# Optimization experiments

Measured on AMD Instinct MI355X. Metric: run time of the kernel, lower is better.

## Reference

```python
import jax, jax.numpy as jnp
import numpy as np

D = 256  # model dim, used for 1/sqrt(d) scaling


def setup_inputs() -> dict:
    key = jax.random.key(0)
    ks = jax.random.split(key, 6)
    B, N, Dm, K = 4, 8192, 256, 256
    s = 0.02
    return {
        "I": jax.random.normal(ks[0], (B, N, Dm), dtype=jnp.float32),
        "Wq": jax.random.normal(ks[1], (Dm, Dm), dtype=jnp.float32) * s,
        "Wk": jax.random.normal(ks[2], (Dm, Dm), dtype=jnp.float32) * s,
        "Wv": jax.random.normal(ks[3], (Dm, Dm), dtype=jnp.float32) * s,
        "We": jax.random.normal(ks[4], (K, N), dtype=jnp.float32) * s,
        "Wf": jax.random.normal(ks[5], (K, N), dtype=jnp.float32) * s,
    }


def reference(I, Wq, Wk, Wv, We, Wf):
    # I: [B, n, d]; nn.Linear applies x @ W.T
    Q = jnp.einsum("bnd,ed->bne", I, Wq)          # [B, n, d]
    K = jnp.einsum("bnd,ed->bne", I, Wk)          # [B, n, d]
    V = jnp.einsum("bnd,ed->bne", I, Wv)          # [B, n, d]
    # E projects K along the sequence axis: K^T [B,d,n] -> [B,d,k]
    Ke = jnp.einsum("bnd,kn->bdk", K, We)         # [B, d, k]
    # F projects V along the sequence axis, then transpose back: [B,k,d]
    Vf = jnp.einsum("bnd,kn->bkd", V, Wf)         # [B, k, d]
    scale = 1.0 / jnp.sqrt(jnp.asarray(D, dtype=Q.dtype))
    PBar = jnp.einsum("bnd,bdk->bnk", Q, Ke) * scale  # [B, n, k]
    PBar = jax.nn.softmax(PBar, axis=2)
    # dropout omitted (eval / deterministic reference)
    Head = jnp.einsum("bnk,bkd->bnd", PBar, Vf)   # [B, n, d]
    return Head
```

## Files before the change

### kernel.cpp

```cpp
#include <hip/hip_runtime.h>
#include <stdint.h>


typedef unsigned short u16;
typedef __attribute__((ext_vector_type(8))) __bf16 bf16x8;
typedef __attribute__((ext_vector_type(4))) float f32x4;
typedef __attribute__((ext_vector_type(4))) unsigned short u16x4;
typedef __attribute__((ext_vector_type(8))) unsigned short u16x8;

__device__ __forceinline__ u16 f2bf(float f) {
  union { __bf16 h; u16 u; } v;
  v.h = (__bf16)f;
  return v.u;
}

__device__ __forceinline__ void gld_lds16(const void* g, void* l) {
  __builtin_amdgcn_global_load_lds((const __attribute__((address_space(1))) void*)g,
                                   (__attribute__((address_space(3))) void*)l, 16, 0, 0);
}

__device__ __forceinline__ void stage_tile(const u16* src, long long ld, long long kb,
                                           u16* lds, int tid) {
#pragma unroll
  for (int r = 0; r < 4; ++r) {
    const int off = r * 4096 + tid * 16;
    const int row = off >> 7;
    const int colb = (off & 127) ^ ((row & 7) << 4);
    gld_lds16(src + (long long)row * ld + kb + (colb >> 1), (char*)lds + off);
  }
}

__device__ __forceinline__ void mfma_step(const u16* Alds, const u16* Blds, int lane, int wr,
                                          int wc, f32x4 (&acc)[4][4]) {
#pragma unroll
  for (int kk = 0; kk < 2; ++kk) {
    const int ko2 = (kk * 32 + (lane >> 4) * 8) * 2;
    bf16x8 a[4], b[4];
#pragma unroll
    for (int m = 0; m < 4; ++m) {
      const int ar = wr + m * 16 + (lane & 15);
      a[m] = *(const bf16x8*)((const char*)Alds + ((ar * 128 + ko2) ^ ((ar & 7) << 4)));
    }
#pragma unroll
    for (int n = 0; n < 4; ++n) {
      const int br = wc + n * 16 + (lane & 15);
      b[n] = *(const bf16x8*)((const char*)Blds + ((br * 128 + ko2) ^ ((br & 7) << 4)));
    }
#pragma unroll
    for (int m = 0; m < 4; ++m)
#pragma unroll
      for (int n = 0; n < 4; ++n)
        acc[m][n] = __builtin_amdgcn_mfma_f32_16x16x32_bf16(a[m], b[n], acc[m][n], 0, 0, 0);
  }
}

__global__ __launch_bounds__(256) void k0(const float* __restrict__ I,
                                          const float* __restrict__ Wq,
                                          const float* __restrict__ Wk,
                                          const float* __restrict__ Wv,
                                          const float* __restrict__ We,
                                          const float* __restrict__ Wf,
                                          u16* __restrict__ Ibf, u16* __restrict__ IT,
                                          u16* __restrict__ WqT, u16* __restrict__ WkT,
                                          u16* __restrict__ WvB, u16* __restrict__ WeB,
                                          u16* __restrict__ WfB) {
  const int p = blockIdx.x, t = threadIdx.x;
  if (p < 2080) {
    __shared__ u16 T[4096];
    const float* src;
    u16 *dT, *dS;
    long long srow, scol, tld;
    if (p < 2048) {
      const int b = p >> 9, id = p & 511;
      src = I + (long long)b * 2097152;
      srow = (long long)(id >> 2) * 64;
      scol = (long long)(id & 3) * 64;
      dS = Ibf + (long long)b * 2097152;
      dT = IT + (long long)b * 2097152;
      tld = 8192;
    } else {
      const int q = p - 2048;
      src = (q < 16) ? Wq : Wk;
      const int id = q & 15;
      srow = (long long)(id >> 2) * 64;
      scol = (long long)(id & 3) * 64;
      dS = nullptr;
      dT = (q < 16) ? WqT : WkT;
      tld = 256;
    }
    const int cc = t & 15, rL = t >> 4;
#pragma unroll
    for (int i = 0; i < 4; ++i) {
      const int r = rL + 16 * i;
      f32x4 v = *(const f32x4*)(src + (srow + r) * 256 + scol + cc * 4);
      u16x4 o = {f2bf(v[0]), f2bf(v[1]), f2bf(v[2]), f2bf(v[3])};
      if (dS) *(u16x4*)(dS + (srow + r) * 256 + scol + cc * 4) = o;
      const int P = (cc + (r & 15) + 4 * (r >> 4)) & 15;
      *(u16x4*)&T[r * 64 + P * 4] = o;
    }
    __syncthreads();
    const int dd = t >> 2, ch2 = t & 3;
    u16 buf[16];
#pragma unroll
    for (int j = 0; j < 16; ++j) {
      const int P = ((dd >> 2) + j + 4 * ch2) & 15;
      buf[j] = T[(ch2 * 16 + j) * 64 + P * 4 + (dd & 3)];
    }
    u16* dp = dT + (scol + dd) * tld + srow + ch2 * 16;
    *(u16x8*)dp = *(u16x8*)&buf[0];
    *(u16x8*)(dp + 8) = *(u16x8*)&buf[8];
  } else {
    const long long base = (long long)(p - 2080) * 4096;
#pragma unroll
    for (int rnd = 0; rnd < 4; ++rnd) {
      const long long e = base + rnd * 1024 + t * 4;
      const float* s;
      u16* d;
      long long eo;
      if (e < 65536) { s = Wv; d = WvB; eo = e; }
      else if (e < 2162688) { s = We; d = WeB; eo = e - 65536; }
      else { s = Wf; d = WfB; eo = e - 2162688; }
      f32x4 v = *(const f32x4*)(s + eo);
      *(u16x4*)(d + eo) = u16x4{f2bf(v[0]), f2bf(v[1]), f2bf(v[2]), f2bf(v[3])};
    }
  }
}

__global__ __launch_bounds__(256) void k1(const u16* __restrict__ WqT,
                                          const u16* __restrict__ WkT,
                                          const u16* __restrict__ WeB,
                                          const u16* __restrict__ WfB,
                                          const u16* __restrict__ IT,
                                          float* __restrict__ Pp, u16* __restrict__ G) {
  __shared__ u16 Alds[2][8192];
  __shared__ u16 Blds[2][8192];
  const int tid = threadIdx.x, lane = tid & 63, w = tid >> 6;
  const int wr = (w >> 1) * 64, wc = (w & 1) * 64;
  const u16 *A, *Bp;
  long long lda, k0, crow, ccol;
  int nkt;
  float* Cf = nullptr;
  u16* Cb = nullptr;
  if (blockIdx.x >= 512) {
    const int tl = blockIdx.x - 512;
    crow = (long long)(tl >> 1) * 128;
    ccol = (long long)(tl & 1) * 128;
    A = WqT + crow * 256;
    Bp = WkT + ccol * 256;
    lda = 256; k0 = 0; nkt = 4;
    Cb = G;
  } else {
    const int l = ((blockIdx.x & 7) << 6) + (blockIdx.x >> 3);
    const int mT = l & 1, nT = (l >> 1) & 1, s = (l >> 2) & 15, b = (l >> 6) & 3, op = l >> 8;
    A = (op ? WfB : WeB) + (long long)mT * 128 * 8192;
    Bp = IT + (long long)b * 2097152 + (long long)nT * 128 * 8192;
    lda = 8192;
    k0 = (long long)s * 512;
    nkt = 8;
    Cf = Pp + ((long long)(op * 4 + b) * 16 + s) * 65536;
    crow = (long long)mT * 128;
    ccol = (long long)nT * 128;
  }

  f32x4 acc[4][4];
#pragma unroll
  for (int m = 0; m < 4; ++m)
#pragma unroll
    for (int n = 0; n < 4; ++n) acc[m][n] = f32x4{0.f, 0.f, 0.f, 0.f};

  stage_tile(A, lda, k0, Alds[0], tid);
  stage_tile(Bp, lda, k0, Blds[0], tid);
  __syncthreads();
  int cur = 0;
  for (int kt = 0; kt < nkt; ++kt) {
    if (kt + 1 < nkt) {
      stage_tile(A, lda, k0 + (kt + 1) * 64, Alds[cur ^ 1], tid);
      stage_tile(Bp, lda, k0 + (kt + 1) * 64, Blds[cur ^ 1], tid);
    }
    mfma_step(Alds[cur], Blds[cur], lane, wr, wc, acc);
    __syncthreads();
    cur ^= 1;
  }

  const int r0 = (lane >> 4) * 4, c0 = lane & 15;
#pragma unroll
  for (int m = 0; m < 4; ++m)
#pragma unroll
    for (int n = 0; n < 4; ++n) {
      const long long row = crow + wr + m * 16 + r0;
      const long long col = ccol + wc + n * 16 + c0;
#pragma unroll
      for (int j = 0; j < 4; ++j) {
        if (Cf) Cf[(row + j) * 256 + col] = acc[m][n][j];
        else Cb[(row + j) * 256 + col] = f2bf(acc[m][n][j]);
      }
    }
}

__global__ __launch_bounds__(256) void reduce16(const float* __restrict__ P,
                                                u16* __restrict__ O) {
  const long long t = (long long)blockIdx.x * 256 + threadIdx.x;
  const long long g = t >> 14;
  const long long e = (t & 16383) << 2;
  const float* p = P + g * 1048576 + e;
  f32x4 s = {0.f, 0.f, 0.f, 0.f};
#pragma unroll
  for (int i = 0; i < 16; ++i) s += *(const f32x4*)(p + i * 65536);
  u16x4 o = {f2bf(s[0]), f2bf(s[1]), f2bf(s[2]), f2bf(s[3])};
  *(u16x4*)(O + g * 65536 + e) = o;
}

__global__ __launch_bounds__(256) void k3(const u16* __restrict__ SS, const u16* __restrict__ G,
                                          const u16* __restrict__ WvB, u16* __restrict__ Me,
                                          u16* __restrict__ VfT) {
  __shared__ u16 Alds[2][8192];
  __shared__ u16 Blds[2][8192];
  const int tid = threadIdx.x, lane = tid & 63, w = tid >> 6;
  const int wr = (w >> 1) * 64, wc = (w & 1) * 64;
  const int u = blockIdx.x;
  const int path = u >> 4, b = (u >> 2) & 3, mT = (u >> 1) & 1, nT = u & 1;
  const u16 *A, *Bp;
  u16* C;
  if (path == 0) { A = SS + b * 65536; Bp = G; C = Me + b * 65536; }
  else { A = WvB; Bp = SS + (4 + b) * 65536; C = VfT + b * 65536; }
  A += (long long)mT * 128 * 256;
  Bp += (long long)nT * 128 * 256;

  f32x4 acc[4][4];
#pragma unroll
  for (int m = 0; m < 4; ++m)
#pragma unroll
    for (int n = 0; n < 4; ++n) acc[m][n] = f32x4{0.f, 0.f, 0.f, 0.f};

  stage_tile(A, 256, 0, Alds[0], tid);
  stage_tile(Bp, 256, 0, Blds[0], tid);
  __syncthreads();
  int cur = 0;
  for (int kt = 0; kt < 4; ++kt) {
    if (kt + 1 < 4) {
      stage_tile(A, 256, (kt + 1) * 64, Alds[cur ^ 1], tid);
      stage_tile(Bp, 256, (kt + 1) * 64, Blds[cur ^ 1], tid);
    }
    mfma_step(Alds[cur], Blds[cur], lane, wr, wc, acc);
    __syncthreads();
    cur ^= 1;
  }

  const int r0 = (lane >> 4) * 4, c0 = lane & 15;
#pragma unroll
  for (int m = 0; m < 4; ++m)
#pragma unroll
    for (int n = 0; n < 4; ++n) {
      const int row = mT * 128 + wr + m * 16 + r0;
      const int col = nT * 128 + wc + n * 16 + c0;
#pragma unroll
      for (int j = 0; j < 4; ++j) C[(row + j) * 256 + col] = f2bf(acc[m][n][j]);
    }
}

__device__ __forceinline__ void stage_bs(const u16* src, u16* Bs, int tid) {
#pragma unroll
  for (int r = 0; r < 8; ++r) {
    const int off = r * 4096 + tid * 16;
    const int row = off >> 7;
    const int colb = (off & 127) ^ ((row & 7) << 4);
    gld_lds16(src + row * 256 + (colb >> 1), (char*)Bs + off);
  }
}

__global__ __launch_bounds__(256) void flash3(const u16* __restrict__ Q,
                                              const u16* __restrict__ KeT,
                                              const u16* __restrict__ VfT,
                                              float* __restrict__ out) {
  __shared__ u16 Qs[16384];
  __shared__ u16 Bs[16384];
  __shared__ float Ms[256];
  __shared__ float Ss[256];
  const int tid = threadIdx.x;
  const int lane = tid & 63;
  const int w = tid >> 6;
  const int wc = w * 64;
  const int l = ((blockIdx.x & 7) << 6) + (blockIdx.x >> 3);
  const long long R0 = (long long)l * 64;
  const int batch = (int)(R0 >> 13);
  const u16* KeTb = KeT + (long long)batch * 65536;
  const u16* VfTb = VfT + (long long)batch * 65536;
  const int r0 = (lane >> 4) * 4, c0 = lane & 15;

#pragma unroll
  for (int r = 0; r < 8; ++r) {
    const int off = r * 4096 + tid * 16;
    const int row = off >> 9;
    const int colb = (off & 511) ^ ((row & 7) << 4);
    gld_lds16(Q + (R0 + row) * 256 + (colb >> 1), (char*)Qs + off);
  }

  f32x4 acc[4][4];
#pragma unroll
  for (int m = 0; m < 4; ++m)
#pragma unroll
    for (int n = 0; n < 4; ++n) acc[m][n] = f32x4{0.f, 0.f, 0.f, 0.f};

  for (int kc = 0; kc < 4; ++kc) {
    __syncthreads();
    stage_bs(KeTb + kc * 64, Bs, tid);
    __syncthreads();
#pragma unroll
    for (int kk = 0; kk < 2; ++kk) {
      const int ko = kk * 32 + (lane >> 4) * 8;
      bf16x8 a[4], b[4];
#pragma unroll
      for (int m = 0; m < 4; ++m) {
        const int ar = m * 16 + (lane & 15);
        a[m] = *(const bf16x8*)((const char*)Qs +
                                ((ar * 512 + (kc * 64 + ko) * 2) ^ ((ar & 7) << 4)));
      }
#pragma unroll
      for (int n = 0; n < 4; ++n) {
        const int br = wc + n * 16 + (lane & 15);
        b[n] = *(const bf16x8*)((const char*)Bs + ((br * 128 + ko * 2) ^ ((br & 7) << 4)));
      }
#pragma unroll
      for (int m = 0; m < 4; ++m)
#pragma unroll
        for (int n = 0; n < 4; ++n)
          acc[m][n] = __builtin_amdgcn_mfma_f32_16x16x32_bf16(a[m], b[n], acc[m][n], 0, 0, 0);
    }
  }

  float red[4][4];
#pragma unroll
  for (int m = 0; m < 4; ++m)
#pragma unroll
    for (int j = 0; j < 4; ++j)
      red[m][j] = fmaxf(fmaxf(acc[m][0][j], acc[m][1][j]), fmaxf(acc[m][2][j], acc[m][3][j]));
#pragma unroll
  for (int d = 1; d < 16; d <<= 1)
#pragma unroll
    for (int m = 0; m < 4; ++m)
#pragma unroll
      for (int j = 0; j < 4; ++j) red[m][j] = fmaxf(red[m][j], __shfl_xor(red[m][j], d));
  if ((lane & 15) == 0) {
#pragma unroll
    for (int m = 0; m < 4; ++m)
#pragma unroll
      for (int j = 0; j < 4; ++j) Ms[(m * 16 + r0 + j) * 4 + w] = red[m][j];
  }
  __syncthreads();
  float gm[4][4];
#pragma unroll
  for (int m = 0; m < 4; ++m)
#pragma unroll
    for (int j = 0; j < 4; ++j) {
      const f32x4 t = *(const f32x4*)&Ms[(m * 16 + r0 + j) * 4];
      gm[m][j] = fmaxf(fmaxf(t[0], t[1]), fmaxf(t[2], t[3]));
    }
#pragma unroll
  for (int m = 0; m < 4; ++m)
#pragma unroll
    for (int j = 0; j < 4; ++j) {
      float s = 0.f;
#pragma unroll
      for (int n = 0; n < 4; ++n) {
        const float e = __expf((acc[m][n][j] - gm[m][j]) * 0.0625f);
        acc[m][n][j] = e;
        s += e;
      }
      red[m][j] = s;
    }
#pragma unroll
  for (int d = 1; d < 16; d <<= 1)
#pragma unroll
    for (int m = 0; m < 4; ++m)
#pragma unroll
      for (int j = 0; j < 4; ++j) red[m][j] += __shfl_xor(red[m][j], d);
  if ((lane & 15) == 0) {
#pragma unroll
    for (int m = 0; m < 4; ++m)
#pragma unroll
      for (int j = 0; j < 4; ++j) Ss[(m * 16 + r0 + j) * 4 + w] = red[m][j];
  }
  __syncthreads();
#pragma unroll
  for (int m = 0; m < 4; ++m)
#pragma unroll
    for (int j = 0; j < 4; ++j) {
      const int row = m * 16 + r0 + j;
      const f32x4 t = *(const f32x4*)&Ss[row * 4];
      const float inv = 1.0f / (t[0] + t[1] + t[2] + t[3]);
#pragma unroll
      for (int n = 0; n < 4; ++n) {
        const int col = wc + n * 16 + c0;
        *(u16*)((char*)Qs + ((row * 512 + col * 2) ^ ((row & 7) << 4))) =
            f2bf(acc[m][n][j] * inv);
      }
    }
#pragma unroll
  for (int m = 0; m < 4; ++m)
#pragma unroll
    for (int n = 0; n < 4; ++n) acc[m][n] = f32x4{0.f, 0.f, 0.f, 0.f};

  for (int kc = 0; kc < 4; ++kc) {
    __syncthreads();
    stage_bs(VfTb + kc * 64, Bs, tid);
    __syncthreads();
#pragma unroll
    for (int kk = 0; kk < 2; ++kk) {
      const int ko = kk * 32 + (lane >> 4) * 8;
      bf16x8 a[4], b[4];
#pragma unroll
      for (int m = 0; m < 4; ++m) {
        const int ar = m * 16 + (lane & 15);
        a[m] = *(const bf16x8*)((const char*)Qs +
                                ((ar * 512 + (kc * 64 + ko) * 2) ^ ((ar & 7) << 4)));
      }
#pragma unroll
      for (int n = 0; n < 4; ++n) {
        const int br = wc + n * 16 + (lane & 15);
        b[n] = *(const bf16x8*)((const char*)Bs + ((br * 128 + ko * 2) ^ ((br & 7) << 4)));
      }
#pragma unroll
      for (int m = 0; m < 4; ++m)
#pragma unroll
        for (int n = 0; n < 4; ++n)
          acc[m][n] = __builtin_amdgcn_mfma_f32_16x16x32_bf16(a[m], b[n], acc[m][n], 0, 0, 0);
    }
  }

#pragma unroll
  for (int m = 0; m < 4; ++m)
#pragma unroll
    for (int n = 0; n < 4; ++n) {
      const long long row = R0 + m * 16 + r0;
      const int col = wc + n * 16 + c0;
#pragma unroll
      for (int j = 0; j < 4; ++j) out[(row + j) * 256 + col] = acc[m][n][j];
    }
}

extern "C" void kernel_launch(void* const* d_in, const int* in_sizes, int n_in, void* d_out,
                              int out_size, void* d_ws, size_t ws_size, hipStream_t stream) {
  (void)in_sizes; (void)n_in; (void)out_size; (void)ws_size;
  const float* I  = (const float*)d_in[0];
  const float* Wq = (const float*)d_in[1];
  const float* Wk = (const float*)d_in[2];
  const float* Wv = (const float*)d_in[3];
  const float* We = (const float*)d_in[4];
  const float* Wf = (const float*)d_in[5];
  float* out = (float*)d_out;
  char* ws = (char*)d_ws;

  u16* Ibf  = (u16*)(ws + 0);
  u16* IT   = (u16*)(ws + 16777216);
  u16* WqT  = (u16*)(ws + 33554432);
  u16* WkT  = (u16*)(ws + 33685504);
  u16* WvB  = (u16*)(ws + 33816576);
  u16* WeB  = (u16*)(ws + 33947648);
  u16* WfB  = (u16*)(ws + 38141952);
  u16* G    = (u16*)(ws + 42336256);
  float* Pp = (float*)(ws + 42467328);
  u16* SS   = (u16*)(ws + 76021760);
  u16* Me   = (u16*)(ws + 77070336);
  u16* VfT  = (u16*)(ws + 77594624);

  k0<<<3120, 256, 0, stream>>>(I, Wq, Wk, Wv, We, Wf, Ibf, IT, WqT, WkT, WvB, WeB, WfB);
  k1<<<516, 256, 0, stream>>>(WqT, WkT, WeB, WfB, IT, Pp, G);
  reduce16<<<512, 256, 0, stream>>>(Pp, SS);
  k3<<<32, 256, 0, stream>>>(SS, G, WvB, Me, VfT);
  flash3<<<512, 256, 0, stream>>>(Ibf, Me, VfT, out);
}
```

Baseline: 173.2 us.

## Double-buffer Ke/Vf tiles in fused attention kernel with larger 128-row blocks

The final attention kernel now handles 128 rows per block using 512 threads (8 waves in a 2x4 grid) instead of 64 rows with 256 threads. The projected-key and projected-value tiles are double-buffered, so the next chunk's async global-to-LDS load overlaps the MFMA work on the current chunk, and the first Vf chunk is prefetched during the softmax. Each block starts its k-chunk loop at a different offset to spread L2 traffic. The trade-offs are more LDS per block (about 132 KB), which limits occupancy, and a halved grid of 256 blocks.

```diff
diff --git a/kernel.cpp b/kernel.cpp
--- a/kernel.cpp
+++ b/kernel.cpp
@@ -258,42 +258,72 @@
     }
 }
 
-__device__ __forceinline__ void stage_bs(const u16* src, u16* Bs, int tid) {
-#pragma unroll
-  for (int r = 0; r < 8; ++r) {
-    const int off = r * 4096 + tid * 16;
+
+__device__ __forceinline__ void stage_p(const u16* src, u16* dst, int tid) {
+#pragma unroll
+  for (int r = 0; r < 4; ++r) {
+    const int off = r * 8192 + tid * 16;
     const int row = off >> 7;
     const int colb = (off & 127) ^ ((row & 7) << 4);
-    gld_lds16(src + row * 256 + (colb >> 1), (char*)Bs + off);
-  }
-}
-
-__global__ __launch_bounds__(256) void flash3(const u16* __restrict__ Q,
-                                              const u16* __restrict__ KeT,
+    gld_lds16(src + row * 256 + (colb >> 1), (char*)dst + off);
+  }
+}
+
+__device__ __forceinline__ void mfma8(const u16* Qs, const u16* Bsb, int lane, int wr, int wc,
+                                      int kc, f32x4 (&acc)[4][4]) {
+#pragma unroll
+  for (int kk = 0; kk < 2; ++kk) {
+    const int ko = kk * 32 + (lane >> 4) * 8;
+    bf16x8 a[4], b[4];
+#pragma unroll
+    for (int m = 0; m < 4; ++m) {
+      const int ar = wr + m * 16 + (lane & 15);
+      a[m] = *(const bf16x8*)((const char*)Qs +
+                              ((ar * 512 + (kc * 64 + ko) * 2) ^ ((ar & 7) << 4)));
+    }
+#pragma unroll
+    for (int n = 0; n < 4; ++n) {
+      const int br = wc + n * 16 + (lane & 15);
+      b[n] = *(const bf16x8*)((const char*)Bsb + ((br * 128 + ko * 2) ^ ((br & 7) << 4)));
+    }
+#pragma unroll
+    for (int m = 0; m < 4; ++m)
+#pragma unroll
+      for (int n = 0; n < 4; ++n)
+        acc[m][n] = __builtin_amdgcn_mfma_f32_16x16x32_bf16(a[m], b[n], acc[m][n], 0, 0, 0);
+  }
+}
+
+__global__ __launch_bounds__(512) void flash4(const u16* __restrict__ Q,
+                                              const u16* __restrict__ Me,
                                               const u16* __restrict__ VfT,
                                               float* __restrict__ out) {
-  __shared__ u16 Qs[16384];
-  __shared__ u16 Bs[16384];
-  __shared__ float Ms[256];
-  __shared__ float Ss[256];
+  __shared__ u16 Qs[32768];
+  __shared__ u16 Bs[2][16384];
+  __shared__ float Ms[512];
+  __shared__ float Ss[512];
   const int tid = threadIdx.x;
   const int lane = tid & 63;
   const int w = tid >> 6;
-  const int wc = w * 64;
-  const int l = ((blockIdx.x & 7) << 6) + (blockIdx.x >> 3);
-  const long long R0 = (long long)l * 64;
-  const int batch = (int)(R0 >> 13);
-  const u16* KeTb = KeT + (long long)batch * 65536;
-  const u16* VfTb = VfT + (long long)batch * 65536;
+  const int wr = (w & 1) * 64;
+  const int wcg = w >> 1;
+  const int wc = wcg * 64;
+  const int l = ((blockIdx.x & 7) << 5) + (blockIdx.x >> 3);
+  const long long R0 = (long long)l * 128;
+  const int batch = l >> 6;
+  const int kc0 = l & 3;
+  const u16* Meb = Me + (long long)batch * 65536;
+  const u16* Vfb = VfT + (long long)batch * 65536;
   const int r0 = (lane >> 4) * 4, c0 = lane & 15;
 
 #pragma unroll
   for (int r = 0; r < 8; ++r) {
-    const int off = r * 4096 + tid * 16;
+    const int off = r * 8192 + tid * 16;
     const int row = off >> 9;
     const int colb = (off & 511) ^ ((row & 7) << 4);
     gld_lds16(Q + (R0 + row) * 256 + (colb >> 1), (char*)Qs + off);
   }
+  stage_p(Meb + kc0 * 64, Bs[0], tid);
 
   f32x4 acc[4][4];
 #pragma unroll
@@ -301,31 +331,13 @@
 #pragma unroll
     for (int n = 0; n < 4; ++n) acc[m][n] = f32x4{0.f, 0.f, 0.f, 0.f};
 
-  for (int kc = 0; kc < 4; ++kc) {
+  int cur = 0;
+#pragma unroll
+  for (int i = 0; i < 4; ++i) {
     __syncthreads();
-    stage_bs(KeTb + kc * 64, Bs, tid);
-    __syncthreads();
-#pragma unroll
-    for (int kk = 0; kk < 2; ++kk) {
-      const int ko = kk * 32 + (lane >> 4) * 8;
-      bf16x8 a[4], b[4];
-#pragma unroll
-      for (int m = 0; m < 4; ++m) {
-        const int ar = m * 16 + (lane & 15);
-        a[m] = *(const bf16x8*)((const char*)Qs +
-                                ((ar * 512 + (kc * 64 + ko) * 2) ^ ((ar & 7) << 4)));
-      }
-#pragma unroll
-      for (int n = 0; n < 4; ++n) {
-        const int br = wc + n * 16 + (lane & 15);
-        b[n] = *(const bf16x8*)((const char*)Bs + ((br * 128 + ko * 2) ^ ((br & 7) << 4)));
-      }
-#pragma unroll
-      for (int m = 0; m < 4; ++m)
-#pragma unroll
-        for (int n = 0; n < 4; ++n)
-          acc[m][n] = __builtin_amdgcn_mfma_f32_16x16x32_bf16(a[m], b[n], acc[m][n], 0, 0, 0);
-    }
+    if (i < 3) stage_p(Meb + (((kc0 + i + 1) & 3)) * 64, Bs[cur ^ 1], tid);
+    mfma8(Qs, Bs[cur], lane, wr, wc, (kc0 + i) & 3, acc);
+    cur ^= 1;
   }
 
   float red[4][4];
@@ -340,11 +352,12 @@
     for (int m = 0; m < 4; ++m)
 #pragma unroll
       for (int j = 0; j < 4; ++j) red[m][j] = fmaxf(red[m][j], __shfl_xor(red[m][j], d));
+  stage_p(Vfb + kc0 * 64, Bs[0], tid);
   if ((lane & 15) == 0) {
 #pragma unroll
     for (int m = 0; m < 4; ++m)
 #pragma unroll
-      for (int j = 0; j < 4; ++j) Ms[(m * 16 + r0 + j) * 4 + w] = red[m][j];
+      for (int j = 0; j < 4; ++j) Ms[(wr + m * 16 + r0 + j) * 4 + wcg] = red[m][j];
   }
   __syncthreads();
   float gm[4][4];
@@ -352,7 +365,7 @@
   for (int m = 0; m < 4; ++m)
 #pragma unroll
     for (int j = 0; j < 4; ++j) {
-      const f32x4 t = *(const f32x4*)&Ms[(m * 16 + r0 + j) * 4];
+      const f32x4 t = *(const f32x4*)&Ms[(wr + m * 16 + r0 + j) * 4];
       gm[m][j] = fmaxf(fmaxf(t[0], t[1]), fmaxf(t[2], t[3]));
     }
 #pragma unroll
@@ -378,14 +391,14 @@
 #pragma unroll
     for (int m = 0; m < 4; ++m)
 #pragma unroll
-      for (int j = 0; j < 4; ++j) Ss[(m * 16 + r0 + j) * 4 + w] = red[m][j];
+      for (int j = 0; j < 4; ++j) Ss[(wr + m * 16 + r0 + j) * 4 + wcg] = red[m][j];
   }
   __syncthreads();
 #pragma unroll
   for (int m = 0; m < 4; ++m)
 #pragma unroll
     for (int j = 0; j < 4; ++j) {
-      const int row = m * 16 + r0 + j;
+      const int row = wr + m * 16 + r0 + j;
       const f32x4 t = *(const f32x4*)&Ss[row * 4];
       const float inv = 1.0f / (t[0] + t[1] + t[2] + t[3]);
 #pragma unroll
@@ -400,38 +413,20 @@
 #pragma unroll
     for (int n = 0; n < 4; ++n) acc[m][n] = f32x4{0.f, 0.f, 0.f, 0.f};
 
-  for (int kc = 0; kc < 4; ++kc) {
+  cur = 0;
+#pragma unroll
+  for (int i = 0; i < 4; ++i) {
     __syncthreads();
-    stage_bs(VfTb + kc * 64, Bs, tid);
-    __syncthreads();
-#pragma unroll
-    for (int kk = 0; kk < 2; ++kk) {
-      const int ko = kk * 32 + (lane >> 4) * 8;
-      bf16x8 a[4], b[4];
-#pragma unroll
-      for (int m = 0; m < 4; ++m) {
-        const int ar = m * 16 + (lane & 15);
-        a[m] = *(const bf16x8*)((const char*)Qs +
-                                ((ar * 512 + (kc * 64 + ko) * 2) ^ ((ar & 7) << 4)));
-      }
-#pragma unroll
-      for (int n = 0; n < 4; ++n) {
-        const int br = wc + n * 16 + (lane & 15);
-        b[n] = *(const bf16x8*)((const char*)Bs + ((br * 128 + ko * 2) ^ ((br & 7) << 4)));
-      }
-#pragma unroll
-      for (int m = 0; m < 4; ++m)
-#pragma unroll
-        for (int n = 0; n < 4; ++n)
-          acc[m][n] = __builtin_amdgcn_mfma_f32_16x16x32_bf16(a[m], b[n], acc[m][n], 0, 0, 0);
-    }
+    if (i < 3) stage_p(Vfb + (((kc0 + i + 1) & 3)) * 64, Bs[cur ^ 1], tid);
+    mfma8(Qs, Bs[cur], lane, wr, wc, (kc0 + i) & 3, acc);
+    cur ^= 1;
   }
 
 #pragma unroll
   for (int m = 0; m < 4; ++m)
 #pragma unroll
     for (int n = 0; n < 4; ++n) {
-      const long long row = R0 + m * 16 + r0;
+      const long long row = R0 + wr + m * 16 + r0;
       const int col = wc + n * 16 + c0;
 #pragma unroll
       for (int j = 0; j < 4; ++j) out[(row + j) * 256 + col] = acc[m][n][j];
@@ -467,5 +462,5 @@
   k1<<<516, 256, 0, stream>>>(WqT, WkT, WeB, WfB, IT, Pp, G);
   reduce16<<<512, 256, 0, stream>>>(Pp, SS);
   k3<<<32, 256, 0, stream>>>(SS, G, WvB, Me, VfT);
-  flash3<<<512, 256, 0, stream>>>(Ibf, Me, VfT, out);
-}
+  flash4<<<256, 512, 0, stream>>>(Ibf, Me, VfT, out);
+}
```

After: 163.6 us. 1.06x faster.

## Stage per-wave B strips to drop block barriers in flash kernel

Applied to the files above, without the earlier changes.

Each wave now stages only its own 64-row strip of the Me/VfT operand into a private LDS buffer, so the two __syncthreads per k-chunk become a per-wave vmcnt wait. K-chunk iteration order is also rotated per block (kc0 = l & 3), which spreads global reads across different parts of the matrices. The change removes block-wide synchronization stalls, but each wave now waits on its own loads with no prefetch overlap.

```diff
diff --git a/kernel.cpp b/kernel.cpp
--- a/kernel.cpp
+++ b/kernel.cpp
@@ -258,22 +258,12 @@
     }
 }
 
-__device__ __forceinline__ void stage_bs(const u16* src, u16* Bs, int tid) {
-#pragma unroll
-  for (int r = 0; r < 8; ++r) {
-    const int off = r * 4096 + tid * 16;
-    const int row = off >> 7;
-    const int colb = (off & 127) ^ ((row & 7) << 4);
-    gld_lds16(src + row * 256 + (colb >> 1), (char*)Bs + off);
-  }
-}
-
-__global__ __launch_bounds__(256) void flash3(const u16* __restrict__ Q,
-                                              const u16* __restrict__ KeT,
+__global__ __launch_bounds__(256) void flash6(const u16* __restrict__ Q,
+                                              const u16* __restrict__ Me,
                                               const u16* __restrict__ VfT,
                                               float* __restrict__ out) {
   __shared__ u16 Qs[16384];
-  __shared__ u16 Bs[16384];
+  __shared__ u16 Bst[4][4096];
   __shared__ float Ms[256];
   __shared__ float Ss[256];
   const int tid = threadIdx.x;
@@ -283,8 +273,9 @@
   const int l = ((blockIdx.x & 7) << 6) + (blockIdx.x >> 3);
   const long long R0 = (long long)l * 64;
   const int batch = (int)(R0 >> 13);
-  const u16* KeTb = KeT + (long long)batch * 65536;
-  const u16* VfTb = VfT + (long long)batch * 65536;
+  const int kc0 = l & 3;
+  const u16* Meb = Me + (long long)batch * 65536;
+  const u16* Vfb = VfT + (long long)batch * 65536;
   const int r0 = (lane >> 4) * 4, c0 = lane & 15;
 
 #pragma unroll
@@ -294,6 +285,19 @@
     const int colb = (off & 511) ^ ((row & 7) << 4);
     gld_lds16(Q + (R0 + row) * 256 + (colb >> 1), (char*)Qs + off);
   }
+  __syncthreads();
+
+  auto stage_strip = [&](const u16* base, int kc) {
+#pragma unroll
+    for (int r = 0; r < 8; ++r) {
+      const int off = r * 1024 + lane * 16;
+      const int row = off >> 7;
+      const int colb = (off & 127) ^ ((row & 7) << 4);
+      gld_lds16(base + (wc + row) * 256 + kc * 64 + (colb >> 1), (char*)Bst[w] + off);
+    }
+    asm volatile("s_waitcnt vmcnt(0)" ::: "memory");
+    __builtin_amdgcn_sched_barrier(0);
+  };
 
   f32x4 acc[4][4];
 #pragma unroll
@@ -301,10 +305,9 @@
 #pragma unroll
     for (int n = 0; n < 4; ++n) acc[m][n] = f32x4{0.f, 0.f, 0.f, 0.f};
 
-  for (int kc = 0; kc < 4; ++kc) {
-    __syncthreads();
-    stage_bs(KeTb + kc * 64, Bs, tid);
-    __syncthreads();
+  for (int i = 0; i < 4; ++i) {
+    const int kc = (kc0 + i) & 3;
+    stage_strip(Meb, kc);
 #pragma unroll
     for (int kk = 0; kk < 2; ++kk) {
       const int ko = kk * 32 + (lane >> 4) * 8;
@@ -317,8 +320,8 @@
       }
 #pragma unroll
       for (int n = 0; n < 4; ++n) {
-        const int br = wc + n * 16 + (lane & 15);
-        b[n] = *(const bf16x8*)((const char*)Bs + ((br * 128 + ko * 2) ^ ((br & 7) << 4)));
+        const int br = n * 16 + (lane & 15);
+        b[n] = *(const bf16x8*)((const char*)Bst[w] + ((br * 128 + ko * 2) ^ ((br & 7) << 4)));
       }
 #pragma unroll
       for (int m = 0; m < 4; ++m)
@@ -399,11 +402,11 @@
   for (int m = 0; m < 4; ++m)
 #pragma unroll
     for (int n = 0; n < 4; ++n) acc[m][n] = f32x4{0.f, 0.f, 0.f, 0.f};
-
-  for (int kc = 0; kc < 4; ++kc) {
-    __syncthreads();
-    stage_bs(VfTb + kc * 64, Bs, tid);
-    __syncthreads();
+  __syncthreads();
+
+  for (int i = 0; i < 4; ++i) {
+    const int kc = (kc0 + i) & 3;
+    stage_strip(Vfb, kc);
 #pragma unroll
     for (int kk = 0; kk < 2; ++kk) {
       const int ko = kk * 32 + (lane >> 4) * 8;
@@ -416,8 +419,8 @@
       }
 #pragma unroll
       for (int n = 0; n < 4; ++n) {
-        const int br = wc + n * 16 + (lane & 15);
-        b[n] = *(const bf16x8*)((const char*)Bs + ((br * 128 + ko * 2) ^ ((br & 7) << 4)));
+        const int br = n * 16 + (lane & 15);
+        b[n] = *(const bf16x8*)((const char*)Bst[w] + ((br * 128 + ko * 2) ^ ((br & 7) << 4)));
       }
 #pragma unroll
       for (int m = 0; m < 4; ++m)
@@ -467,5 +470,5 @@
   k1<<<516, 256, 0, stream>>>(WqT, WkT, WeB, WfB, IT, Pp, G);
   reduce16<<<512, 256, 0, stream>>>(Pp, SS);
   k3<<<32, 256, 0, stream>>>(SS, G, WvB, Me, VfT);
-  flash3<<<512, 256, 0, stream>>>(Ibf, Me, VfT, out);
-}
+  flash6<<<512, 256, 0, stream>>>(Ibf, Me, VfT, out);
+}
```

New measurement: 162.9 us. 6.0% less time.
